# Optimization experiments

Measured on AMD Instinct MI355X. Metric: run time of the kernel, lower is better.

## Reference

```python
import jax, jax.numpy as jnp
import numpy as np

N_USER = 150000
N_RECIPE = 150000
H = 64        # hidden_channels
UF = 58       # user_feat_dim
RF = 128      # recipe_feat_dim
E = 2000000   # rating edges
EL = 500000   # supervision edges


def _lin(k, fan_out, fan_in):
    s = 1.0 / np.sqrt(fan_in)
    kw, kb = jax.random.split(k)
    w = jax.random.uniform(kw, (fan_out, fan_in), jnp.float32, -s, s)
    b = jax.random.uniform(kb, (fan_out,), jnp.float32, -s, s)
    return w, b


def setup_inputs() -> dict:
    key = jax.random.key(0)
    ks = jax.random.split(key, 16)
    inp = {
        'x_user': jax.random.normal(ks[0], (N_USER, UF), jnp.float32),
        'x_recipe': jax.random.normal(ks[1], (N_RECIPE, RF), jnp.float32),
        'user_node_id': jnp.arange(N_USER, dtype=jnp.int64 if jax.config.jax_enable_x64 else jnp.int32),
        'recipe_node_id': jnp.arange(N_RECIPE, dtype=jnp.int64 if jax.config.jax_enable_x64 else jnp.int32),
        'edge_index': jax.random.randint(ks[2], (2, E), 0, N_USER),
        'edge_label_index': jax.random.randint(ks[3], (2, EL), 0, N_USER),
    }
    inp['user_lin_w'], inp['user_lin_b'] = _lin(ks[4], H, UF)
    inp['recipe_lin_w'], inp['recipe_lin_b'] = _lin(ks[5], H, RF)
    inp['user_emb'] = jax.random.normal(ks[6], (N_USER, H), jnp.float32)
    inp['recipe_emb'] = jax.random.normal(ks[7], (N_RECIPE, H), jnp.float32)
    # SAGEConv per layer (1,2) per relation (rates: user->recipe, rev: recipe->user)
    i = 8
    for layer in (1, 2):
        for rel in ('rates', 'rev'):
            wl, bl = _lin(ks[i], H, H)
            wr, _ = _lin(ks[i + 1], H, H)  # lin_r has no bias in PyG SAGEConv
            inp[f'c{layer}_{rel}_wl'] = wl
            inp[f'c{layer}_{rel}_bl'] = bl
            inp[f'c{layer}_{rel}_wr'] = wr
            i += 2
    return inp


def sage_conv(x_src, x_dst, src, dst, wl, bl, wr, n_dst):
    # PyG SAGEConv: lin_l(mean of neighbor messages) + lin_r(self)
    msg = x_src[src]                                              # [E, H] gather
    summed = jax.ops.segment_sum(msg, dst, num_segments=n_dst)    # [n_dst, H]
    cnt = jax.ops.segment_sum(jnp.ones((src.shape[0],), x_src.dtype), dst,
                              num_segments=n_dst)
    mean = summed / jnp.maximum(cnt, 1.0)[:, None]
    return mean @ wl.T + bl + x_dst @ wr.T


def reference(x_user, x_recipe, user_node_id, recipe_node_id, edge_index,
              edge_label_index, user_lin_w, user_lin_b, recipe_lin_w,
              recipe_lin_b, user_emb, recipe_emb,
              c1_rates_wl, c1_rates_bl, c1_rates_wr,
              c1_rev_wl, c1_rev_bl, c1_rev_wr,
              c2_rates_wl, c2_rates_bl, c2_rates_wr,
              c2_rev_wl, c2_rev_bl, c2_rev_wr):
    # Input encoders: linear + embedding lookup
    xu = x_user @ user_lin_w.T + user_lin_b + user_emb[user_node_id]
    xr = x_recipe @ recipe_lin_w.T + recipe_lin_b + recipe_emb[recipe_node_id]

    u_src, r_dst = edge_index[0], edge_index[1]

    # Layer 1 (hetero: each node type receives from exactly one relation)
    hr = sage_conv(xu, xr, u_src, r_dst, c1_rates_wl, c1_rates_bl, c1_rates_wr, N_RECIPE)
    hu = sage_conv(xr, xu, r_dst, u_src, c1_rev_wl, c1_rev_bl, c1_rev_wr, N_USER)
    hu, hr = jax.nn.relu(hu), jax.nn.relu(hr)

    # Layer 2
    hr2 = sage_conv(hu, hr, u_src, r_dst, c2_rates_wl, c2_rates_bl, c2_rates_wr, N_RECIPE)
    hu2 = sage_conv(hr, hu, r_dst, u_src, c2_rev_wl, c2_rev_bl, c2_rev_wr, N_USER)

    # Dot-product edge classifier
    return (hu2[edge_label_index[0]] * hr2[edge_label_index[1]]).sum(axis=-1)
```

## Files before the change

kernel.cpp:

```cpp
#include <hip/hip_runtime.h>
#include <hip/hip_fp16.h>

constexpr int NU = 150000;
constexpr int NR = 150000;
constexpr int Hc = 64;
constexpr int UF = 58;
constexpr int RF = 128;
constexpr long EE = 2000000;
constexpr long ELc = 500000;
constexpr int NTOT = NU + NR;
constexpr int BKT = 256;
constexpr int NB_R = (NR + BKT - 1) / BKT;
constexpr int NB_U = (NU + BKT - 1) / BKT;
constexpr int NBKT = NB_R + NB_U;
constexpr int CAP = 4096;
constexpr int CHUNK = 4096;
constexpr int NCHUNK = (int)((EE + CHUNK - 1) / CHUNK);
constexpr int NTILE = NU / 16;
constexpr int GB8 = (NU / 8 + 3) / 4;

typedef _Float16 f16;
typedef f16 f16x8 __attribute__((ext_vector_type(8)));
typedef float f32x4 __attribute__((ext_vector_type(4)));

__global__ void init_bcur_kernel(int* __restrict__ bcur) {
    int i = blockIdx.x * blockDim.x + threadIdx.x;
    if (i < NBKT) bcur[i] = i * CAP;
}

__global__ void scatter_records_kernel(const int* __restrict__ ei, int* __restrict__ bcur,
                                       int* __restrict__ rec) {
    __shared__ int lc[NBKT];
    for (int i = threadIdx.x; i < NBKT; i += 256) lc[i] = 0;
    __syncthreads();
    long e0 = (long)blockIdx.x * CHUNK;
    for (int k = threadIdx.x; k < CHUNK; k += 256) {
        long e = e0 + k;
        if (e < EE) {
            int u = ei[e], r = ei[EE + e];
            atomicAdd(&lc[r >> 8], 1);
            atomicAdd(&lc[NB_R + (u >> 8)], 1);
        }
    }
    __syncthreads();
    for (int i = threadIdx.x; i < NBKT; i += 256) {
        int c = lc[i];
        lc[i] = c ? atomicAdd(&bcur[i], c) : 0;
    }
    __syncthreads();
    for (int k = threadIdx.x; k < CHUNK; k += 256) {
        long e = e0 + k;
        if (e < EE) {
            int u = ei[e], r = ei[EE + e];
            int p1 = atomicAdd(&lc[r >> 8], 1);
            rec[p1] = ((r & 255) << 18) | u;
            int p2 = atomicAdd(&lc[NB_R + (u >> 8)], 1);
            rec[p2] = ((u & 255) << 18) | r;
        }
    }
}

__global__ void build_adj_kernel(const int* __restrict__ rec, const int* __restrict__ bcur,
                                 int* __restrict__ adj, int* __restrict__ base,
                                 int* __restrict__ cnt) {
    __shared__ int c256[BKT];
    __shared__ int off256[BKT];
    int b = blockIdx.x;
    int s = b * CAP, e = bcur[b];
    int t = threadIdx.x;
    c256[t] = 0;
    __syncthreads();
    for (int k = s + t; k < e; k += 256) atomicAdd(&c256[rec[k] >> 18], 1);
    __syncthreads();
    int v = c256[t];
    off256[t] = v;
    __syncthreads();
    for (int off = 1; off < 256; off <<= 1) {
        int x = (t >= off) ? off256[t - off] : 0;
        __syncthreads();
        off256[t] += x;
        __syncthreads();
    }
    int excl = off256[t] - v;
    bool isU = (b >= NB_R);
    int node = (isU ? (b - NB_R) : b) * BKT + t;
    int lim = isU ? NU : NR;
    if (node < lim) {
        int cid = isU ? (NR + node) : node;
        base[cid] = s + excl;
        cnt[cid] = v;
    }
    c256[t] = s + excl;
    __syncthreads();
    for (int k = s + t; k < e; k += 256) {
        int rv = rec[k];
        int p = atomicAdd(&c256[rv >> 18], 1);
        adj[p] = rv & 0x3FFFF;
    }
}

template <int F>
__global__ __launch_bounds__(256) void encode_mfma(
        const float* __restrict__ xin, const float* __restrict__ w,
        const float* __restrict__ b, const float* __restrict__ emb,
        const int* __restrict__ nid, __half* __restrict__ out) {
    constexpr int KT = (F + 31) / 32;
    __shared__ f16 wlds[Hc * F];
    for (int i = threadIdx.x; i < Hc * F; i += 256) wlds[i] = (f16)w[i];
    __syncthreads();
    int l = threadIdx.x & 63;
    int m = l & 15;
    int g = l >> 4;
    f16x8 bf[4][KT];
#pragma unroll
    for (int ct = 0; ct < 4; ++ct)
#pragma unroll
        for (int kt = 0; kt < KT; ++kt)
#pragma unroll
            for (int j = 0; j < 8; ++j) {
                int k = kt * 32 + g * 8 + j;
                bf[ct][kt][j] = (k < F) ? wlds[(ct * 16 + m) * F + k] : (f16)0.0f;
            }
    float bv[4];
#pragma unroll
    for (int ct = 0; ct < 4; ++ct) bv[ct] = b[ct * 16 + m];
    int wid0 = (int)(((long)blockIdx.x * 256 + threadIdx.x) >> 6);
    int nw = (gridDim.x * 256) >> 6;
    for (int rt = wid0; rt < NTILE; rt += nw) {
        int r0 = rt * 16;
        const float* xrow = xin + (long)(r0 + m) * F;
        f16x8 af[KT];
#pragma unroll
        for (int kt = 0; kt < KT; ++kt)
#pragma unroll
            for (int jj = 0; jj < 4; ++jj) {
                int k = kt * 32 + g * 8 + jj * 2;
                if (k + 1 < F) {
                    float2 v = *(const float2*)(xrow + k);
                    af[kt][jj * 2] = (f16)v.x;
                    af[kt][jj * 2 + 1] = (f16)v.y;
                } else {
                    af[kt][jj * 2] = (k < F) ? (f16)xrow[k] : (f16)0.0f;
                    af[kt][jj * 2 + 1] = (f16)0.0f;
                }
            }
        f32x4 acc[4] = {{0,0,0,0},{0,0,0,0},{0,0,0,0},{0,0,0,0}};
#pragma unroll
        for (int ct = 0; ct < 4; ++ct)
#pragma unroll
            for (int kt = 0; kt < KT; ++kt)
                acc[ct] = __builtin_amdgcn_mfma_f32_16x16x32_f16(af[kt], bf[ct][kt], acc[ct], 0, 0, 0);
#pragma unroll
        for (int q = 0; q < 4; ++q) {
            int r = r0 + g * 4 + q;
            long ebase = (long)nid[r] * Hc;
#pragma unroll
            for (int ct = 0; ct < 4; ++ct) {
                int col = ct * 16 + m;
                float v = acc[ct][q] + bv[ct] + emb[ebase + col];
                out[(long)r * Hc + col] = __float2half(v);
            }
        }
    }
}

__global__ __launch_bounds__(256) void dense2_mfma(
        const __half* inU, const float* wlU, const float* brU, const float* wrU,
        __half* ToutU, __half* PREU,
        const __half* inR, const float* wlR, const float* brR, const float* wrR,
        __half* ToutR, __half* PRER) {
    __shared__ f16 wlds[2][Hc * Hc];
    int half = gridDim.x >> 1;
    bool isR = blockIdx.x >= half;
    const __half* in = isR ? inR : inU;
    const float* wl = isR ? wlR : wlU;
    const float* wr = isR ? wrR : wrU;
    const float* br = isR ? brR : brU;
    __half* Tout = isR ? ToutR : ToutU;
    __half* PRE  = isR ? PRER : PREU;
    for (int i = threadIdx.x; i < Hc * Hc; i += 256) {
        wlds[0][i] = (f16)wl[i];
        wlds[1][i] = (f16)wr[i];
    }
    __syncthreads();
    int l = threadIdx.x & 63;
    int m = l & 15;
    int g = l >> 4;
    f16x8 bf[8][2];
#pragma unroll
    for (int ct = 0; ct < 4; ++ct)
#pragma unroll
        for (int kt = 0; kt < 2; ++kt) {
            bf[ct][kt]     = *(const f16x8*)&wlds[0][(ct * 16 + m) * Hc + kt * 32 + g * 8];
            bf[4 + ct][kt] = *(const f16x8*)&wlds[1][(ct * 16 + m) * Hc + kt * 32 + g * 8];
        }
    float bv[4];
#pragma unroll
    for (int ct = 0; ct < 4; ++ct) bv[ct] = br[ct * 16 + m];
    int wid0 = (int)((((long)blockIdx.x - (isR ? half : 0)) * 256 + threadIdx.x) >> 6);
    int nw = (half * 256) >> 6;
    for (int rt = wid0; rt < NTILE; rt += nw) {
        int r0 = rt * 16;
        f16x8 af[2];
        const __half* irow = in + (long)(r0 + m) * Hc;
        af[0] = *(const f16x8*)(irow + g * 8);
        af[1] = *(const f16x8*)(irow + 32 + g * 8);
        f32x4 acc[8] = {{0,0,0,0},{0,0,0,0},{0,0,0,0},{0,0,0,0},
                        {0,0,0,0},{0,0,0,0},{0,0,0,0},{0,0,0,0}};
#pragma unroll
        for (int ct = 0; ct < 8; ++ct)
#pragma unroll
            for (int kt = 0; kt < 2; ++kt)
                acc[ct] = __builtin_amdgcn_mfma_f32_16x16x32_f16(af[kt], bf[ct][kt], acc[ct], 0, 0, 0);
#pragma unroll
        for (int q = 0; q < 4; ++q) {
            int r = r0 + g * 4 + q;
#pragma unroll
            for (int ct = 0; ct < 4; ++ct) {
                int col = ct * 16 + m;
                Tout[(long)r * Hc + col] = __float2half(acc[ct][q]);
                PRE[(long)r * Hc + col] = __float2half(acc[4 + ct][q] + bv[ct]);
            }
        }
    }
}

__global__ __launch_bounds__(256) void gather8_kernel(
        const __half* __restrict__ TA, __half* __restrict__ ioA,
        const __half* __restrict__ TB, __half* __restrict__ ioB,
        const int* __restrict__ base, const int* __restrict__ cnt,
        const int* __restrict__ adj, int relu) {
    int l = threadIdx.x & 63;
    int d = l >> 3;
    int o = l & 7;
    int half = gridDim.x >> 1;
    bool isU = blockIdx.x >= half;
    int bid = blockIdx.x - (isU ? half : 0);
    int wid = bid * 4 + (threadIdx.x >> 6);
    int r = wid * 8 + d;
    if (r >= NU) return;
    int noff = isU ? NR : 0;
    const __half* T = isU ? TB : TA;
    __half* io = isU ? ioB : ioA;
    int b0 = base[noff + r], c = cnt[noff + r];
    int co = o * 8;
    __half* op = io + (long)r * Hc + co;
    uint4 cur = *(const uint4*)op;
    __half2 z = __float2half2_rn(0.0f);
    __half2 s0 = z, s1 = z, s2 = z, s3 = z;
    __half2 t0 = z, t1 = z, t2 = z, t3 = z;
    __half2 u0 = z, u1 = z, u2 = z, u3 = z;
    __half2 w0 = z, w1 = z, w2 = z, w3 = z;
    int j = 0;
    for (; j + 3 < c; j += 4) {
        int n0 = adj[b0 + j];
        int n1 = adj[b0 + j + 1];
        int n2 = adj[b0 + j + 2];
        int n3 = adj[b0 + j + 3];
        uint4 v0 = *(const uint4*)(T + n0 * Hc + co);
        uint4 v1 = *(const uint4*)(T + n1 * Hc + co);
        uint4 v2 = *(const uint4*)(T + n2 * Hc + co);
        uint4 v3 = *(const uint4*)(T + n3 * Hc + co);
        s0 = __hadd2(s0, *(__half2*)&v0.x); t0 = __hadd2(t0, *(__half2*)&v1.x);
        u0 = __hadd2(u0, *(__half2*)&v2.x); w0 = __hadd2(w0, *(__half2*)&v3.x);
        s1 = __hadd2(s1, *(__half2*)&v0.y); t1 = __hadd2(t1, *(__half2*)&v1.y);
        u1 = __hadd2(u1, *(__half2*)&v2.y); w1 = __hadd2(w1, *(__half2*)&v3.y);
        s2 = __hadd2(s2, *(__half2*)&v0.z); t2 = __hadd2(t2, *(__half2*)&v1.z);
        u2 = __hadd2(u2, *(__half2*)&v2.z); w2 = __hadd2(w2, *(__half2*)&v3.z);
        s3 = __hadd2(s3, *(__half2*)&v0.w); t3 = __hadd2(t3, *(__half2*)&v1.w);
        u3 = __hadd2(u3, *(__half2*)&v2.w); w3 = __hadd2(w3, *(__half2*)&v3.w);
    }
    for (; j < c; ++j) {
        int n = adj[b0 + j];
        uint4 v = *(const uint4*)(T + n * Hc + co);
        s0 = __hadd2(s0, *(__half2*)&v.x);
        s1 = __hadd2(s1, *(__half2*)&v.y);
        s2 = __hadd2(s2, *(__half2*)&v.z);
        s3 = __hadd2(s3, *(__half2*)&v.w);
    }
    s0 = __hadd2(__hadd2(s0, t0), __hadd2(u0, w0));
    s1 = __hadd2(__hadd2(s1, t1), __hadd2(u1, w1));
    s2 = __hadd2(__hadd2(s2, t2), __hadd2(u2, w2));
    s3 = __hadd2(__hadd2(s3, t3), __hadd2(u3, w3));
    float inv = 1.0f / fmaxf((float)c, 1.0f);
    __half2 acc[4] = {s0, s1, s2, s3};
    unsigned int* cw = &cur.x;
    uint4 outv;
    unsigned int* ow = &outv.x;
#pragma unroll
    for (int q = 0; q < 4; ++q) {
        float2 f = __half22float2(*(__half2*)&cw[q]);
        float2 a = __half22float2(acc[q]);
        float ox = f.x + a.x * inv;
        float oy = f.y + a.y * inv;
        if (relu) { ox = fmaxf(ox, 0.0f); oy = fmaxf(oy, 0.0f); }
        __half2 h = __floats2half2_rn(ox, oy);
        ow[q] = *(unsigned int*)&h;
    }
    *(uint4*)op = outv;
}

__global__ void edge_dot_kernel(const int* __restrict__ eli,
                                const __half* __restrict__ HU2, const __half* __restrict__ HR2,
                                float* __restrict__ out) {
    long gid = (long)blockIdx.x * blockDim.x + threadIdx.x;
    long e = gid >> 4;
    int t = (int)(gid & 15);
    if (e >= ELc) return;
    int a = eli[e], b = eli[ELc + e];
    const __half2* xa = (const __half2*)(HU2 + (long)a * Hc + t * 4);
    const __half2* yb = (const __half2*)(HR2 + (long)b * Hc + t * 4);
    float2 x0 = __half22float2(xa[0]), x1 = __half22float2(xa[1]);
    float2 y0 = __half22float2(yb[0]), y1 = __half22float2(yb[1]);
    float v = x0.x * y0.x + x0.y * y0.y + x1.x * y1.x + x1.y * y1.y;
    v += __shfl_xor(v, 1);
    v += __shfl_xor(v, 2);
    v += __shfl_xor(v, 4);
    v += __shfl_xor(v, 8);
    if (t == 0) out[e] = v;
}

extern "C" void kernel_launch(void* const* d_in, const int* in_sizes, int n_in,
                              void* d_out, int out_size, void* d_ws, size_t ws_size,
                              hipStream_t stream) {
    const float* x_user   = (const float*)d_in[0];
    const float* x_recipe = (const float*)d_in[1];
    const int*   user_nid = (const int*)d_in[2];
    const int*   rec_nid  = (const int*)d_in[3];
    const int*   edge_index = (const int*)d_in[4];
    const int*   edge_label = (const int*)d_in[5];
    const float* u_w   = (const float*)d_in[6];
    const float* u_b   = (const float*)d_in[7];
    const float* r_w   = (const float*)d_in[8];
    const float* r_b   = (const float*)d_in[9];
    const float* u_emb = (const float*)d_in[10];
    const float* r_emb = (const float*)d_in[11];
    const float* c1ra_wl = (const float*)d_in[12];
    const float* c1ra_bl = (const float*)d_in[13];
    const float* c1ra_wr = (const float*)d_in[14];
    const float* c1rv_wl = (const float*)d_in[15];
    const float* c1rv_bl = (const float*)d_in[16];
    const float* c1rv_wr = (const float*)d_in[17];
    const float* c2ra_wl = (const float*)d_in[18];
    const float* c2ra_bl = (const float*)d_in[19];
    const float* c2ra_wr = (const float*)d_in[20];
    const float* c2rv_wl = (const float*)d_in[21];
    const float* c2rv_bl = (const float*)d_in[22];
    const float* c2rv_wr = (const float*)d_in[23];

    const long NH = (long)NU * Hc;
    __half* B0 = (__half*)d_ws;
    __half* B1 = B0 + NH;
    __half* B2 = B1 + NH;
    __half* B3 = B2 + NH;
    __half* TAh = B3 + NH;
    __half* TBh = TAh + NH;
    int* cnt   = (int*)(TBh + NH);
    int* base  = cnt + NTOT;
    int* bcur  = base + NTOT;
    int* adj   = bcur + NBKT;
    int* rec = (int*)B2;

    init_bcur_kernel<<<(NBKT + 255) / 256, 256, 0, stream>>>(bcur);
    scatter_records_kernel<<<NCHUNK, 256, 0, stream>>>(edge_index, bcur, rec);
    build_adj_kernel<<<NBKT, 256, 0, stream>>>(rec, bcur, adj, base, cnt);

    encode_mfma<UF><<<1024, 256, 0, stream>>>(x_user, u_w, u_b, u_emb, user_nid, B0);
    encode_mfma<RF><<<1024, 256, 0, stream>>>(x_recipe, r_w, r_b, r_emb, rec_nid, B1);

    dense2_mfma<<<2048, 256, 0, stream>>>(
        B0, c1ra_wl, c1rv_bl, c1rv_wr, TAh, B2,
        B1, c1rv_wl, c1ra_bl, c1ra_wr, TBh, B3);

    gather8_kernel<<<2 * GB8, 256, 0, stream>>>(TAh, B3, TBh, B2, base, cnt, adj, 1);

    dense2_mfma<<<2048, 256, 0, stream>>>(
        B2, c2ra_wl, c2rv_bl, c2rv_wr, TAh, B0,
        B3, c2rv_wl, c2ra_bl, c2ra_wr, TBh, B1);

    gather8_kernel<<<2 * GB8, 256, 0, stream>>>(TAh, B1, TBh, B0, base, cnt, adj, 0);

    edge_dot_kernel<<<(ELc * 16) / 256, 256, 0, stream>>>(edge_label, B0, B1, (float*)d_out);
}
```

Baseline: 387.5 us.

## Store hidden features in column-octet-major layout for gather locality

Dense outputs are now stored as eight planes, each holding an 8-wide column slice for all nodes. The gather kernel gives each thread one node and one plane, with blocks split by plane, so each pass gathers from a 2.4 MB slice that is meant to stay cache-resident. The dense layer-2 input path and the edge-dot kernel are adapted to read this layout. The cost is strided, scattered stores in the dense kernel, four separate gather launches instead of two, and a one-thread-per-node mapping whose per-thread loop length varies with node degree.

```diff
diff --git a/kernel.cpp b/kernel.cpp
--- a/kernel.cpp
+++ b/kernel.cpp
@@ -17,7 +17,8 @@
 constexpr int CHUNK = 4096;
 constexpr int NCHUNK = (int)((EE + CHUNK - 1) / CHUNK);
 constexpr int NTILE = NU / 16;
-constexpr int GB8 = (NU / 8 + 3) / 4;
+constexpr long N8 = (long)NU * 8;
+constexpr int GOCT = 8 * ((NU + 255) / 256);
 
 typedef _Float16 f16;
 typedef f16 f16x8 __attribute__((ext_vector_type(8)));
@@ -110,7 +111,7 @@
     __syncthreads();
     int l = threadIdx.x & 63;
     int m = l & 15;
-    int g = l >> 4;
+    int gl = l >> 4;
     f16x8 bf[4][KT];
 #pragma unroll
     for (int ct = 0; ct < 4; ++ct)
@@ -118,7 +119,7 @@
         for (int kt = 0; kt < KT; ++kt)
 #pragma unroll
             for (int j = 0; j < 8; ++j) {
-                int k = kt * 32 + g * 8 + j;
+                int k = kt * 32 + gl * 8 + j;
                 bf[ct][kt][j] = (k < F) ? wlds[(ct * 16 + m) * F + k] : (f16)0.0f;
             }
     float bv[4];
@@ -134,7 +135,7 @@
         for (int kt = 0; kt < KT; ++kt)
 #pragma unroll
             for (int jj = 0; jj < 4; ++jj) {
-                int k = kt * 32 + g * 8 + jj * 2;
+                int k = kt * 32 + gl * 8 + jj * 2;
                 if (k + 1 < F) {
                     float2 v = *(const float2*)(xrow + k);
                     af[kt][jj * 2] = (f16)v.x;
@@ -152,7 +153,7 @@
                 acc[ct] = __builtin_amdgcn_mfma_f32_16x16x32_f16(af[kt], bf[ct][kt], acc[ct], 0, 0, 0);
 #pragma unroll
         for (int q = 0; q < 4; ++q) {
-            int r = r0 + g * 4 + q;
+            int r = r0 + gl * 4 + q;
             long ebase = (long)nid[r] * Hc;
 #pragma unroll
             for (int ct = 0; ct < 4; ++ct) {
@@ -164,6 +165,7 @@
     }
 }
 
+template <int GMIN>
 __global__ __launch_bounds__(256) void dense2_mfma(
         const __half* inU, const float* wlU, const float* brU, const float* wrU,
         __half* ToutU, __half* PREU,
@@ -185,14 +187,14 @@
     __syncthreads();
     int l = threadIdx.x & 63;
     int m = l & 15;
-    int g = l >> 4;
+    int gl = l >> 4;
     f16x8 bf[8][2];
 #pragma unroll
     for (int ct = 0; ct < 4; ++ct)
 #pragma unroll
         for (int kt = 0; kt < 2; ++kt) {
-            bf[ct][kt]     = *(const f16x8*)&wlds[0][(ct * 16 + m) * Hc + kt * 32 + g * 8];
-            bf[4 + ct][kt] = *(const f16x8*)&wlds[1][(ct * 16 + m) * Hc + kt * 32 + g * 8];
+            bf[ct][kt]     = *(const f16x8*)&wlds[0][(ct * 16 + m) * Hc + kt * 32 + gl * 8];
+            bf[4 + ct][kt] = *(const f16x8*)&wlds[1][(ct * 16 + m) * Hc + kt * 32 + gl * 8];
         }
     float bv[4];
 #pragma unroll
@@ -202,9 +204,14 @@
     for (int rt = wid0; rt < NTILE; rt += nw) {
         int r0 = rt * 16;
         f16x8 af[2];
-        const __half* irow = in + (long)(r0 + m) * Hc;
-        af[0] = *(const f16x8*)(irow + g * 8);
-        af[1] = *(const f16x8*)(irow + 32 + g * 8);
+#pragma unroll
+        for (int kt = 0; kt < 2; ++kt) {
+            if (GMIN) {
+                af[kt] = *(const f16x8*)(in + (long)(kt * 4 + gl) * N8 + (long)(r0 + m) * 8);
+            } else {
+                af[kt] = *(const f16x8*)(in + (long)(r0 + m) * Hc + kt * 32 + gl * 8);
+            }
+        }
         f32x4 acc[8] = {{0,0,0,0},{0,0,0,0},{0,0,0,0},{0,0,0,0},
                         {0,0,0,0},{0,0,0,0},{0,0,0,0},{0,0,0,0}};
 #pragma unroll
@@ -214,37 +221,28 @@
                 acc[ct] = __builtin_amdgcn_mfma_f32_16x16x32_f16(af[kt], bf[ct][kt], acc[ct], 0, 0, 0);
 #pragma unroll
         for (int q = 0; q < 4; ++q) {
-            int r = r0 + g * 4 + q;
+            int r = r0 + gl * 4 + q;
 #pragma unroll
             for (int ct = 0; ct < 4; ++ct) {
-                int col = ct * 16 + m;
-                Tout[(long)r * Hc + col] = __float2half(acc[ct][q]);
-                PRE[(long)r * Hc + col] = __float2half(acc[4 + ct][q] + bv[ct]);
-            }
-        }
-    }
-}
-
-__global__ __launch_bounds__(256) void gather8_kernel(
-        const __half* __restrict__ TA, __half* __restrict__ ioA,
-        const __half* __restrict__ TB, __half* __restrict__ ioB,
+                long go = (long)(2 * ct + (m >> 3)) * N8 + (long)r * 8 + (m & 7);
+                Tout[go] = __float2half(acc[ct][q]);
+                PRE[go] = __float2half(acc[4 + ct][q] + bv[ct]);
+            }
+        }
+    }
+}
+
+__global__ __launch_bounds__(256) void gather_oct_kernel(
+        const __half* __restrict__ T, __half* __restrict__ io,
         const int* __restrict__ base, const int* __restrict__ cnt,
-        const int* __restrict__ adj, int relu) {
-    int l = threadIdx.x & 63;
-    int d = l >> 3;
-    int o = l & 7;
-    int half = gridDim.x >> 1;
-    bool isU = blockIdx.x >= half;
-    int bid = blockIdx.x - (isU ? half : 0);
-    int wid = bid * 4 + (threadIdx.x >> 6);
-    int r = wid * 8 + d;
+        const int* __restrict__ adj, int noff, int relu) {
+    int g = blockIdx.x & 7;
+    int chunk = blockIdx.x >> 3;
+    int r = chunk * 256 + (int)threadIdx.x;
     if (r >= NU) return;
-    int noff = isU ? NR : 0;
-    const __half* T = isU ? TB : TA;
-    __half* io = isU ? ioB : ioA;
     int b0 = base[noff + r], c = cnt[noff + r];
-    int co = o * 8;
-    __half* op = io + (long)r * Hc + co;
+    const __half* Tg = T + (long)g * N8;
+    __half* op = io + (long)g * N8 + (long)r * 8;
     uint4 cur = *(const uint4*)op;
     __half2 z = __float2half2_rn(0.0f);
     __half2 s0 = z, s1 = z, s2 = z, s3 = z;
@@ -257,10 +255,10 @@
         int n1 = adj[b0 + j + 1];
         int n2 = adj[b0 + j + 2];
         int n3 = adj[b0 + j + 3];
-        uint4 v0 = *(const uint4*)(T + n0 * Hc + co);
-        uint4 v1 = *(const uint4*)(T + n1 * Hc + co);
-        uint4 v2 = *(const uint4*)(T + n2 * Hc + co);
-        uint4 v3 = *(const uint4*)(T + n3 * Hc + co);
+        uint4 v0 = *(const uint4*)(Tg + (long)n0 * 8);
+        uint4 v1 = *(const uint4*)(Tg + (long)n1 * 8);
+        uint4 v2 = *(const uint4*)(Tg + (long)n2 * 8);
+        uint4 v3 = *(const uint4*)(Tg + (long)n3 * 8);
         s0 = __hadd2(s0, *(__half2*)&v0.x); t0 = __hadd2(t0, *(__half2*)&v1.x);
         u0 = __hadd2(u0, *(__half2*)&v2.x); w0 = __hadd2(w0, *(__half2*)&v3.x);
         s1 = __hadd2(s1, *(__half2*)&v0.y); t1 = __hadd2(t1, *(__half2*)&v1.y);
@@ -272,7 +270,7 @@
     }
     for (; j < c; ++j) {
         int n = adj[b0 + j];
-        uint4 v = *(const uint4*)(T + n * Hc + co);
+        uint4 v = *(const uint4*)(Tg + (long)n * 8);
         s0 = __hadd2(s0, *(__half2*)&v.x);
         s1 = __hadd2(s1, *(__half2*)&v.y);
         s2 = __hadd2(s2, *(__half2*)&v.z);
@@ -304,19 +302,22 @@
                                 const __half* __restrict__ HU2, const __half* __restrict__ HR2,
                                 float* __restrict__ out) {
     long gid = (long)blockIdx.x * blockDim.x + threadIdx.x;
-    long e = gid >> 4;
-    int t = (int)(gid & 15);
+    long e = gid >> 3;
+    int t = (int)(gid & 7);
     if (e >= ELc) return;
     int a = eli[e], b = eli[ELc + e];
-    const __half2* xa = (const __half2*)(HU2 + (long)a * Hc + t * 4);
-    const __half2* yb = (const __half2*)(HR2 + (long)b * Hc + t * 4);
-    float2 x0 = __half22float2(xa[0]), x1 = __half22float2(xa[1]);
-    float2 y0 = __half22float2(yb[0]), y1 = __half22float2(yb[1]);
-    float v = x0.x * y0.x + x0.y * y0.y + x1.x * y1.x + x1.y * y1.y;
+    const __half2* xa = (const __half2*)(HU2 + (long)t * N8 + (long)a * 8);
+    const __half2* yb = (const __half2*)(HR2 + (long)t * N8 + (long)b * 8);
+    float v = 0.0f;
+#pragma unroll
+    for (int q = 0; q < 4; ++q) {
+        float2 x = __half22float2(xa[q]);
+        float2 y = __half22float2(yb[q]);
+        v += x.x * y.x + x.y * y.y;
+    }
     v += __shfl_xor(v, 1);
     v += __shfl_xor(v, 2);
     v += __shfl_xor(v, 4);
-    v += __shfl_xor(v, 8);
     if (t == 0) out[e] = v;
 }
 
@@ -368,17 +369,19 @@
     encode_mfma<UF><<<1024, 256, 0, stream>>>(x_user, u_w, u_b, u_emb, user_nid, B0);
     encode_mfma<RF><<<1024, 256, 0, stream>>>(x_recipe, r_w, r_b, r_emb, rec_nid, B1);
 
-    dense2_mfma<<<2048, 256, 0, stream>>>(
+    dense2_mfma<0><<<2048, 256, 0, stream>>>(
         B0, c1ra_wl, c1rv_bl, c1rv_wr, TAh, B2,
         B1, c1rv_wl, c1ra_bl, c1ra_wr, TBh, B3);
 
-    gather8_kernel<<<2 * GB8, 256, 0, stream>>>(TAh, B3, TBh, B2, base, cnt, adj, 1);
-
-    dense2_mfma<<<2048, 256, 0, stream>>>(
+    gather_oct_kernel<<<GOCT, 256, 0, stream>>>(TAh, B3, base, cnt, adj, 0, 1);
+    gather_oct_kernel<<<GOCT, 256, 0, stream>>>(TBh, B2, base, cnt, adj, NR, 1);
+
+    dense2_mfma<1><<<2048, 256, 0, stream>>>(
         B2, c2ra_wl, c2rv_bl, c2rv_wr, TAh, B0,
         B3, c2rv_wl, c2ra_bl, c2ra_wr, TBh, B1);
 
-    gather8_kernel<<<2 * GB8, 256, 0, stream>>>(TAh, B1, TBh, B0, base, cnt, adj, 0);
-
-    edge_dot_kernel<<<(ELc * 16) / 256, 256, 0, stream>>>(edge_label, B0, B1, (float*)d_out);
-}
+    gather_oct_kernel<<<GOCT, 256, 0, stream>>>(TAh, B1, base, cnt, adj, 0, 0);
+    gather_oct_kernel<<<GOCT, 256, 0, stream>>>(TBh, B0, base, cnt, adj, NR, 0);
+
+    edge_dot_kernel<<<(int)((ELc * 8) / 256), 256, 0, stream>>>(edge_label, B0, B1, (float*)d_out);
+}
```

Measured after the change: 721.8 us. 86.3% more time.
